# Kernel tuning notes

Measured on AMD Instinct MI355X. Metric: run time of the kernel, lower is better.

The kernel has to match this reference:

```python
import jax, jax.numpy as jnp
import numpy as np

B, S, D, DO, L, E = 8, 2048, 256, 256, 8, 32768


def setup_inputs() -> dict:
    key = jax.random.key(0)
    k1, k2, k3, k4, k5, k6 = jax.random.split(key, 6)
    node_repr = jax.random.normal(k1, (B, S, D), dtype=jnp.float32)
    edge_src = jax.random.randint(k2, (B, E), 0, S, dtype=jnp.int32)
    edge_tgt = jax.random.randint(k3, (B, E), 0, S, dtype=jnp.int32)
    edge_label = jax.random.randint(k4, (B, E), 0, L, dtype=jnp.int32)
    # per-label Linear params (torch default: kaiming-ish uniform; values here are random stand-ins)
    bound = 1.0 / np.sqrt(D)
    W = jax.random.uniform(k5, (L, D, DO), dtype=jnp.float32, minval=-bound, maxval=bound)
    b = jax.random.uniform(k6, (L, DO), dtype=jnp.float32, minval=-bound, maxval=bound)
    return {"node_repr": node_repr, "edge_src": edge_src, "edge_tgt": edge_tgt,
            "edge_label": edge_label, "W": W, "b": b}


def reference(node_repr, edge_src, edge_tgt, edge_label, W, b):
    # Transform every node by every label's linear once: y[b,l,s,:] = x[b,s,:] @ W[l] + b[l]
    y = jnp.einsum('bsd,ldo->blso', node_repr, W) + b[None, :, None, :]  # [B,L,S,DO]
    bidx = jnp.arange(node_repr.shape[0])[:, None]                       # [B,1]
    msgs = y[bidx, edge_label, edge_src]                                 # [B,E,DO] gather
    out = jnp.zeros(node_repr.shape[:2] + (W.shape[-1],), dtype=node_repr.dtype)
    out = out.at[bidx, edge_tgt].add(msgs)                               # scatter-add into targets
    return jax.nn.relu(out)
```

## Files before the change

kernel.cpp:

```cpp
#include <hip/hip_runtime.h>
#include <stdint.h>

constexpr int NB = 8;
constexpr int NS = 2048;
constexpr int ND = 256;
constexpr int NDO = 256;
constexpr int NL = 8;
constexpr int NE = 32768;
constexpr int K2 = NL * ND;
constexpr int CAP = 32;

typedef __attribute__((ext_vector_type(8))) short bf16x8;
typedef __attribute__((ext_vector_type(4))) float f32x4;
typedef unsigned int u32;

__device__ __forceinline__ float bf2f(uint32_t u) {
    return __uint_as_float(u << 16);
}
__device__ __forceinline__ uint16_t f2bf(float f) {
    uint32_t x = __float_as_uint(f);
    uint32_t r = (x + 0x7fffu + ((x >> 16) & 1u)) >> 16;
    return (uint16_t)r;
}

__device__ __forceinline__ void gl_lds16(const void* gptr, void* lptr) {
    __builtin_amdgcn_global_load_lds(
        (const __attribute__((address_space(1))) u32*)gptr,
        (__attribute__((address_space(3))) u32*)lptr, 16, 0, 0);
}

__global__ __launch_bounds__(256) void part_kernel(
    const float* __restrict__ W, ushort* __restrict__ wt2,
    const int* __restrict__ esrc, const int* __restrict__ etgt,
    const int* __restrict__ elab,
    int* __restrict__ cursor, ushort* __restrict__ bucket) {
    int bid = blockIdx.x;
    int tid = threadIdx.x;
    if (bid < 1024) {
        int b = bid & 7;
        int i = b * NE + (bid >> 3) * 256 + tid;
        int c = (b << 14) + etgt[i] * NL + elab[i];
        int p = atomicAdd(&cursor[c], 1);
        if (p < CAP) bucket[(size_t)c * CAP + p] = (ushort)esrc[i];
    } else {
        __shared__ float tile[64][65];
        int tb = bid - 1024;
        int kt = tb & 31, ot = tb >> 5;
        int k0 = kt * 64, o0 = ot * 64;
        int rr = tid >> 6;
        int cc = tid & 63;
        for (int r16 = 0; r16 < 16; r16++) {
            int row = r16 * 4 + rr;
            tile[row][cc] = W[(size_t)(k0 + row) * NDO + o0 + cc];
        }
        __syncthreads();
        for (int r16 = 0; r16 < 16; r16++) {
            int orow = r16 * 4 + rr;
            wt2[(size_t)(o0 + orow) * K2 + k0 + cc] = f2bf(tile[cc][orow]);
        }
    }
}

__global__ __launch_bounds__(256) void agg_kernel(
    const float* __restrict__ x,
    const int* __restrict__ cursor, const ushort* __restrict__ bucket,
    ushort* __restrict__ Z) {
    int bid = blockIdx.x;
    int b = bid & 7;
    int lane = threadIdx.x & 63;
    int t = (bid >> 3) * 4 + (threadIdx.x >> 6);
    int g = b * NS + t;

    int cv = (lane < 8) ? cursor[(g << 3) + lane] : 0;

    const ushort* bp = bucket + (size_t)g * (NL * CAP);
    int my[4];
#pragma unroll
    for (int c = 0; c < 4; c++) my[c] = bp[c * 64 + lane];

    const float4* x4 = (const float4*)x + (size_t)b * NS * 64;
    ushort* zrow = Z + (size_t)g * K2;

#pragma unroll
    for (int lp = 0; lp < 4; lp++) {
        int n0 = __shfl(cv, 2 * lp);     if (n0 > CAP) n0 = CAP;
        int n1 = __shfl(cv, 2 * lp + 1); if (n1 > CAP) n1 = CAP;
        int ch = my[lp];
        float4 a0 = {0.f, 0.f, 0.f, 0.f};
        float4 a1 = {0.f, 0.f, 0.f, 0.f};
        int nm = (n0 > n1) ? n0 : n1;
        for (int q = 0; q < nm; q++) {
            if (q < n0) {
                int src = __shfl(ch, q);
                float4 v = x4[(size_t)src * 64 + lane];
                a0.x += v.x; a0.y += v.y; a0.z += v.z; a0.w += v.w;
            }
            if (q < n1) {
                int src = __shfl(ch, 32 + q);
                float4 v = x4[(size_t)src * 64 + lane];
                a1.x += v.x; a1.y += v.y; a1.z += v.z; a1.w += v.w;
            }
        }
        ushort4 ob;
        ob.x = f2bf(a0.x); ob.y = f2bf(a0.y); ob.z = f2bf(a0.z); ob.w = f2bf(a0.w);
        ((ushort4*)(zrow + (2 * lp) * ND))[lane] = ob;
        ob.x = f2bf(a1.x); ob.y = f2bf(a1.y); ob.z = f2bf(a1.z); ob.w = f2bf(a1.w);
        ((ushort4*)(zrow + (2 * lp + 1) * ND))[lane] = ob;
    }
}

__global__ __launch_bounds__(256, 4) void gemm2_kernel(
    const ushort* __restrict__ Z, const ushort* __restrict__ wt2,
    const int* __restrict__ cursor, const float* __restrict__ bias,
    float* __restrict__ out) {
    int bid = blockIdx.x;
    int wgid = (bid & 7) * 128 + (bid >> 3);
    int mt = wgid >> 2;
    int n0 = (wgid & 3) * 64;
    int m0 = mt * 64;

    __shared__ ushort As[2][64 * 64];
    __shared__ ushort Bs[2][64 * 64];
    __shared__ int cnt_s[64 * 8];
    __shared__ float bias_s[8 * 64];

    int tid = threadIdx.x;
    int lane = tid & 63;
    int wave = __builtin_amdgcn_readfirstlane(tid >> 6);
    int wm = wave & 1, wn = wave >> 1;
    int ln = lane & 15, quad = lane >> 4;

    {
        int e = tid * 2;
        *(int2*)&cnt_s[e] = *(const int2*)&cursor[(size_t)m0 * 8 + e];
        int l = e >> 6, col = e & 63;
        *(float2*)&bias_s[e] = *(const float2*)&bias[l * NDO + n0 + col];
    }

    const ushort* Ag = Z + (size_t)m0 * K2;
    const ushort* Bg = wt2 + (size_t)n0 * K2;

#define STAGE(buf, k0g)                                                          \
    do {                                                                         \
        _Pragma("unroll")                                                        \
        for (int p = 0; p < 2; p++) {                                            \
            int cid = p * 256 + tid;                                             \
            int r = cid >> 3, ch = (cid & 7) ^ (r & 7);                          \
            gl_lds16(Ag + (size_t)r * K2 + (k0g) + ch * 8,                       \
                     &As[buf][(p * 256 + wave * 64) * 8]);                       \
            gl_lds16(Bg + (size_t)r * K2 + (k0g) + ch * 8,                       \
                     &Bs[buf][(p * 256 + wave * 64) * 8]);                       \
        }                                                                        \
    } while (0)

    f32x4 acc[2][2] = {};

    STAGE(0, 0);
    __syncthreads();

    for (int kt = 0; kt < K2 / 64; kt++) {
        int cur = kt & 1;
        if (kt + 1 < K2 / 64) STAGE(cur ^ 1, (kt + 1) * 64);

#pragma unroll
        for (int ks = 0; ks < 2; ks++) {
            bf16x8 af[2], bfr[2];
#pragma unroll
            for (int i = 0; i < 2; i++) {
                int row = wm * 32 + i * 16 + ln;
                int ci = (ks * 4 + quad) ^ (row & 7);
                af[i] = *(const bf16x8*)&As[cur][row * 64 + ci * 8];
            }
#pragma unroll
            for (int j = 0; j < 2; j++) {
                int row = wn * 32 + j * 16 + ln;
                int ci = (ks * 4 + quad) ^ (row & 7);
                bfr[j] = *(const bf16x8*)&Bs[cur][row * 64 + ci * 8];
            }
#pragma unroll
            for (int i = 0; i < 2; i++)
#pragma unroll
                for (int j = 0; j < 2; j++)
                    acc[i][j] = __builtin_amdgcn_mfma_f32_16x16x32_bf16(
                        af[i], bfr[j], acc[i][j], 0, 0, 0);
        }
        __syncthreads();
    }
#undef STAGE

#pragma unroll
    for (int i = 0; i < 2; i++) {
#pragma unroll
        for (int r = 0; r < 4; r++) {
            int row_l = wm * 32 + i * 16 + quad * 4 + r;
            float cw[8];
#pragma unroll
            for (int l = 0; l < 8; l++) cw[l] = (float)cnt_s[row_l * 8 + l];
#pragma unroll
            for (int j = 0; j < 2; j++) {
                int col_l = wn * 32 + j * 16 + ln;
                float bs = 0.f;
#pragma unroll
                for (int l = 0; l < 8; l++) bs += cw[l] * bias_s[l * 64 + col_l];
                float v = acc[i][j][r] + bs;
                out[(size_t)(m0 + row_l) * NDO + n0 + col_l] = fmaxf(v, 0.f);
            }
        }
    }
}

extern "C" void kernel_launch(void* const* d_in, const int* in_sizes, int n_in,
                              void* d_out, int out_size, void* d_ws, size_t ws_size,
                              hipStream_t stream) {
    const float* x    = (const float*)d_in[0];
    const int*   esrc = (const int*)d_in[1];
    const int*   etgt = (const int*)d_in[2];
    const int*   elab = (const int*)d_in[3];
    const float* W    = (const float*)d_in[4];
    const float* bias = (const float*)d_in[5];
    float* out = (float*)d_out;

    char* ws = (char*)d_ws;
    ushort* wt2    = (ushort*)(ws);
    int*    cursor = (int*)(ws + 1048576);
    ushort* bucket = (ushort*)(ws + 1572864);
    ushort* Z      = (ushort*)(ws + 10485760);

    hipMemsetAsync(cursor, 0, NB * NS * NL * sizeof(int), stream);
    part_kernel<<<1152, 256, 0, stream>>>(W, wt2, esrc, etgt, elab, cursor, bucket);
    agg_kernel<<<4096, 256, 0, stream>>>(x, cursor, bucket, Z);
    gemm2_kernel<<<1024, 256, 0, stream>>>(Z, wt2, cursor, bias, out);
}
```

Measured before the change: 136.6 us.

## Replace double-buffered GEMM staging with single-buffer K=128 tiles; widen bucket to int

The GEMM drops its double-buffered 64-wide K staging in favour of a single 128-wide K tile per iteration with a sync after the loads. This halves the number of barrier pairs but no longer overlaps global loads with MFMA work. The edge bucket storage also changes from 16-bit to 32-bit source indices, which doubles bucket traffic and moves the Z buffer offset. The swizzle only XORs the low 3 bits of the 16-chunk index, which is still a valid permutation.

```diff
diff --git a/kernel.cpp b/kernel.cpp
--- a/kernel.cpp
+++ b/kernel.cpp
@@ -33,7 +33,7 @@
     const float* __restrict__ W, ushort* __restrict__ wt2,
     const int* __restrict__ esrc, const int* __restrict__ etgt,
     const int* __restrict__ elab,
-    int* __restrict__ cursor, ushort* __restrict__ bucket) {
+    int* __restrict__ cursor, int* __restrict__ bucket) {
     int bid = blockIdx.x;
     int tid = threadIdx.x;
     if (bid < 1024) {
@@ -41,7 +41,7 @@
         int i = b * NE + (bid >> 3) * 256 + tid;
         int c = (b << 14) + etgt[i] * NL + elab[i];
         int p = atomicAdd(&cursor[c], 1);
-        if (p < CAP) bucket[(size_t)c * CAP + p] = (ushort)esrc[i];
+        if (p < CAP) bucket[(size_t)c * CAP + p] = esrc[i];
     } else {
         __shared__ float tile[64][65];
         int tb = bid - 1024;
@@ -63,7 +63,7 @@
 
 __global__ __launch_bounds__(256) void agg_kernel(
     const float* __restrict__ x,
-    const int* __restrict__ cursor, const ushort* __restrict__ bucket,
+    const int* __restrict__ cursor, const int* __restrict__ bucket,
     ushort* __restrict__ Z) {
     int bid = blockIdx.x;
     int b = bid & 7;
@@ -73,7 +73,7 @@
 
     int cv = (lane < 8) ? cursor[(g << 3) + lane] : 0;
 
-    const ushort* bp = bucket + (size_t)g * (NL * CAP);
+    const int* bp = bucket + (size_t)g * (NL * CAP);
     int my[4];
 #pragma unroll
     for (int c = 0; c < 4; c++) my[c] = bp[c * 64 + lane];
@@ -119,8 +119,8 @@
     int n0 = (wgid & 3) * 64;
     int m0 = mt * 64;
 
-    __shared__ ushort As[2][64 * 64];
-    __shared__ ushort Bs[2][64 * 64];
+    __shared__ ushort As[64 * 128];
+    __shared__ ushort Bs[64 * 128];
     __shared__ int cnt_s[64 * 8];
     __shared__ float bias_s[8 * 64];
 
@@ -137,45 +137,40 @@
         *(float2*)&bias_s[e] = *(const float2*)&bias[l * NDO + n0 + col];
     }
 
+    f32x4 acc[2][2] = {};
+
     const ushort* Ag = Z + (size_t)m0 * K2;
     const ushort* Bg = wt2 + (size_t)n0 * K2;
 
-#define STAGE(buf, k0g)                                                          \
-    do {                                                                         \
-        _Pragma("unroll")                                                        \
-        for (int p = 0; p < 2; p++) {                                            \
-            int cid = p * 256 + tid;                                             \
-            int r = cid >> 3, ch = (cid & 7) ^ (r & 7);                          \
-            gl_lds16(Ag + (size_t)r * K2 + (k0g) + ch * 8,                       \
-                     &As[buf][(p * 256 + wave * 64) * 8]);                       \
-            gl_lds16(Bg + (size_t)r * K2 + (k0g) + ch * 8,                       \
-                     &Bs[buf][(p * 256 + wave * 64) * 8]);                       \
-        }                                                                        \
-    } while (0)
-
-    f32x4 acc[2][2] = {};
-
-    STAGE(0, 0);
-    __syncthreads();
-
-    for (int kt = 0; kt < K2 / 64; kt++) {
-        int cur = kt & 1;
-        if (kt + 1 < K2 / 64) STAGE(cur ^ 1, (kt + 1) * 64);
-
-#pragma unroll
-        for (int ks = 0; ks < 2; ks++) {
+    for (int k0 = 0; k0 < K2; k0 += 128) {
+#pragma unroll
+        for (int p = 0; p < 4; p++) {
+            int cid = p * 256 + tid;
+            int r = cid >> 4, ch = (cid & 15) ^ (r & 7);
+            gl_lds16(Ag + (size_t)r * K2 + k0 + ch * 8, &As[(p * 256 + wave * 64) * 8]);
+        }
+#pragma unroll
+        for (int p = 0; p < 4; p++) {
+            int cid = p * 256 + tid;
+            int r = cid >> 4, ch = (cid & 15) ^ (r & 7);
+            gl_lds16(Bg + (size_t)r * K2 + k0 + ch * 8, &Bs[(p * 256 + wave * 64) * 8]);
+        }
+        __syncthreads();
+
+#pragma unroll
+        for (int ks = 0; ks < 4; ks++) {
             bf16x8 af[2], bfr[2];
 #pragma unroll
             for (int i = 0; i < 2; i++) {
                 int row = wm * 32 + i * 16 + ln;
                 int ci = (ks * 4 + quad) ^ (row & 7);
-                af[i] = *(const bf16x8*)&As[cur][row * 64 + ci * 8];
+                af[i] = *(const bf16x8*)&As[row * 128 + ci * 8];
             }
 #pragma unroll
             for (int j = 0; j < 2; j++) {
                 int row = wn * 32 + j * 16 + ln;
                 int ci = (ks * 4 + quad) ^ (row & 7);
-                bfr[j] = *(const bf16x8*)&Bs[cur][row * 64 + ci * 8];
+                bfr[j] = *(const bf16x8*)&Bs[row * 128 + ci * 8];
             }
 #pragma unroll
             for (int i = 0; i < 2; i++)
@@ -186,7 +181,6 @@
         }
         __syncthreads();
     }
-#undef STAGE
 
 #pragma unroll
     for (int i = 0; i < 2; i++) {
@@ -223,8 +217,8 @@
     char* ws = (char*)d_ws;
     ushort* wt2    = (ushort*)(ws);
     int*    cursor = (int*)(ws + 1048576);
-    ushort* bucket = (ushort*)(ws + 1572864);
-    ushort* Z      = (ushort*)(ws + 10485760);
+    int*    bucket = (int*)(ws + 1572864);
+    ushort* Z      = (ushort*)(ws + 18350080);
 
     hipMemsetAsync(cursor, 0, NB * NS * NL * sizeof(int), stream);
     part_kernel<<<1152, 256, 0, stream>>>(W, wt2, esrc, etgt, elab, cursor, bucket);
```

Result: no change. 139.3 us (+2.0%).
